# Performance work log

Hardware: AMD Instinct MI355X
Metric: run time of the kernel (lower is better)

## Reference

```python
import jax, jax.numpy as jnp
import numpy as np

B, T, E = 2, 4096, 1024
H = 16
D = E // H  # head_len = 64


def setup_inputs() -> dict:
    key = jax.random.key(0)
    ks = jax.random.split(key, 6)
    s = 1.0 / np.sqrt(E)
    return {
        "x": jax.random.normal(ks[0], (B, T, E), dtype=jnp.float32),
        # torch nn.Linear weights: shape (out, in), y = x @ W.T
        "Wq": jax.random.uniform(ks[1], (E, E), jnp.float32, -s, s),
        "Wk": jax.random.uniform(ks[2], (E, E), jnp.float32, -s, s),
        "Wv": jax.random.uniform(ks[3], (E, E), jnp.float32, -s, s),
        "Wo": jax.random.uniform(ks[4], (E, E), jnp.float32, -s, s),
        "bo": jax.random.uniform(ks[5], (E,), jnp.float32, -s, s),
    }


def reference(x, Wq, Wk, Wv, Wo, bo):
    Bx, Tx, Ex = x.shape
    q = x @ Wq.T
    k = x @ Wk.T
    v = x @ Wv.T
    # (B, T, H, D) -> (B, H, T, D)
    q = q.reshape(Bx, Tx, H, D).transpose(0, 2, 1, 3)
    k = k.reshape(Bx, Tx, H, D).transpose(0, 2, 1, 3)
    v = v.reshape(Bx, Tx, H, D).transpose(0, 2, 1, 3)
    # scores: (B, H, T, T), scaled by sqrt(head_len)
    sim = jnp.einsum("bhqd,bhkd->bhqk", q, k) / jnp.sqrt(jnp.float32(D))
    causal = jnp.tril(jnp.ones((Tx, Tx), dtype=bool))  # True = keep
    sim = jnp.where(causal[None, None], sim, -jnp.inf)
    attn = jax.nn.softmax(sim, axis=-1)
    # dropout_rate = 0.0 (eval) -> identity
    out = jnp.einsum("bhqk,bhkd->bhqd", attn, v)
    out = out.transpose(0, 2, 1, 3).reshape(Bx, Tx, Ex)
    return out @ Wo.T + bo
```

## Files before the change

kernel.cpp:

```cpp
#include <hip/hip_runtime.h>

typedef unsigned short bf16_t;
typedef __bf16 bf16x8 __attribute__((ext_vector_type(8)));
typedef float  v4f   __attribute__((ext_vector_type(4)));

__device__ __forceinline__ bf16_t f2bf(float f) {
    union { float f; unsigned u; } a; a.f = f;
    unsigned r = a.u + 0x7FFFu + ((a.u >> 16) & 1u);
    return (bf16_t)(r >> 16);
}
__device__ __forceinline__ bf16_t f2bf_trunc(float f) {
    union { float f; unsigned u; } a; a.f = f;
    return (bf16_t)(a.u >> 16);
}

#define GL16(g, l) __builtin_amdgcn_global_load_lds( \
    (__attribute__((address_space(1))) void*)(g),    \
    (__attribute__((address_space(3))) void*)(l), 16, 0, 0)

#define QSCALE 0.18033688011f

__global__ __launch_bounds__(256) void cvt_all(
    const float4* __restrict__ x,  const float4* __restrict__ wq,
    const float4* __restrict__ wk, const float4* __restrict__ wv,
    const float4* __restrict__ wo,
    ushort4* __restrict__ xb, ushort4* __restrict__ wqkv, ushort4* __restrict__ wob) {
    int i = blockIdx.x * 256 + threadIdx.x;
    const float4* s; ushort4* d; int off;
    if (i < 2097152) { s = x; d = xb; off = i; }
    else {
        int wdx = (i - 2097152) >> 18;
        off = (i - 2097152) & 262143;
        if      (wdx == 0) { s = wq; d = wqkv; }
        else if (wdx == 1) { s = wk; d = wqkv + 262144; }
        else if (wdx == 2) { s = wv; d = wqkv + 524288; }
        else               { s = wo; d = wob; }
    }
    float4 v = s[off];
    ushort4 o;
    o.x = f2bf(v.x); o.y = f2bf(v.y); o.z = f2bf(v.z); o.w = f2bf(v.w);
    d[off] = o;
}

#define GEMM_MAINLOOP(A_, W_)                                                          \
    __shared__ bf16_t As[128 * 32];                                                    \
    __shared__ bf16_t Bs[128 * 32];                                                    \
    const int tid = threadIdx.x;                                                       \
    const int w = tid >> 6, lane = tid & 63;                                           \
    const int lrow = lane & 15, lq = lane >> 4;                                        \
    const int m0 = blockIdx.y * 128, n0 = blockIdx.x * 128;                            \
    const int srow = w * 16 + (lane >> 2);                                             \
    const int sk = (lane & 3) * 8;                                                     \
    const int wm = (w & 1) * 64, wn = (w >> 1) * 64;                                   \
    v4f acc[4][4];                                                                     \
    _Pragma("unroll") for (int i = 0; i < 4; ++i)                                      \
        _Pragma("unroll") for (int j = 0; j < 4; ++j)                                  \
            acc[i][j] = (v4f){0.f, 0.f, 0.f, 0.f};                                     \
    for (int k0 = 0; k0 < 1024; k0 += 32) {                                            \
        __syncthreads();                                                               \
        GL16(A_ + (size_t)(m0 + srow) * 1024 + k0 + sk,      (char*)As + w * 1024);    \
        GL16(A_ + (size_t)(m0 + 64 + srow) * 1024 + k0 + sk, (char*)As + 4096 + w * 1024); \
        GL16(W_ + (size_t)(n0 + srow) * 1024 + k0 + sk,      (char*)Bs + w * 1024);    \
        GL16(W_ + (size_t)(n0 + 64 + srow) * 1024 + k0 + sk, (char*)Bs + 4096 + w * 1024); \
        __syncthreads();                                                               \
        bf16x8 af[4], bf[4];                                                           \
        _Pragma("unroll") for (int i = 0; i < 4; ++i)                                  \
            af[i] = *(const bf16x8*)&As[(wm + i * 16 + lrow) * 32 + lq * 8];           \
        _Pragma("unroll") for (int j = 0; j < 4; ++j)                                  \
            bf[j] = *(const bf16x8*)&Bs[(wn + j * 16 + lrow) * 32 + lq * 8];           \
        _Pragma("unroll") for (int i = 0; i < 4; ++i)                                  \
            _Pragma("unroll") for (int j = 0; j < 4; ++j)                              \
                acc[i][j] = __builtin_amdgcn_mfma_f32_16x16x32_bf16(af[i], bf[j],      \
                                                                    acc[i][j], 0, 0, 0); \
    }

__global__ __launch_bounds__(256) void gemm_qkv_kernel(
    const bf16_t* __restrict__ A, const bf16_t* __restrict__ W,
    bf16_t* __restrict__ Qb, bf16_t* __restrict__ Kb, bf16_t* __restrict__ Vtb) {
    GEMM_MAINLOOP(A, W)
#pragma unroll
    for (int i = 0; i < 4; ++i)
#pragma unroll
        for (int j = 0; j < 4; ++j)
#pragma unroll
            for (int r = 0; r < 4; ++r) {
                int m = m0 + wm + i * 16 + lq * 4 + r;
                int n = n0 + wn + j * 16 + lrow;
                float v = acc[i][j][r];
                int b = m >> 12, t = m & 4095;
                if (n < 1024) {
                    int h = n >> 6, d = n & 63;
                    Qb[(((size_t)b * 16 + h) * 4096 + t) * 64 + d] = f2bf(v * QSCALE);
                } else if (n < 2048) {
                    int nn = n - 1024, h = nn >> 6, d = nn & 63;
                    Kb[(((size_t)b * 16 + h) * 4096 + t) * 64 + d] = f2bf(v);
                } else {
                    int nn = n - 2048, h = nn >> 6, d = nn & 63;
                    Vtb[(((size_t)b * 16 + h) * 64 + d) * 4096 + t] = f2bf(v);
                }
            }
}

__global__ __launch_bounds__(256) void gemm_out_kernel(
    const bf16_t* __restrict__ A, const bf16_t* __restrict__ W,
    const float* __restrict__ bo, float* __restrict__ out) {
    GEMM_MAINLOOP(A, W)
#pragma unroll
    for (int j = 0; j < 4; ++j) {
        int n = n0 + wn + j * 16 + lrow;
        float bias = bo[n];
#pragma unroll
        for (int i = 0; i < 4; ++i)
#pragma unroll
            for (int r = 0; r < 4; ++r) {
                int m = m0 + wm + i * 16 + lq * 4 + r;
                out[(size_t)m * 1024 + n] = acc[i][j][r] + bias;
            }
    }
}

__global__ __launch_bounds__(256, 2) void attn_kernel(
    const bf16_t* __restrict__ Q, const bf16_t* __restrict__ K,
    const bf16_t* __restrict__ Vt, bf16_t* __restrict__ O) {
    __shared__ bf16_t Kls[2][2][64 * 32];
    __shared__ bf16_t Vls[2][2][64 * 32];
    __shared__ bf16_t Plds[4][32 * 64];
    const int tid = threadIdx.x;
    const int w = tid >> 6, lane = tid & 63;
    const int lrow = lane & 15, lq = lane >> 4;
    const int bh = blockIdx.y;
    const int g = blockIdx.x;

    const bf16_t* Qh = Q + (size_t)bh * (4096 * 64);
    const bf16_t* Kh = K + (size_t)bh * (4096 * 64);
    const bf16_t* Vh = Vt + (size_t)bh * (64 * 4096);
    bf16_t* Pw = Plds[w];
    const int b = bh >> 4, h = bh & 15;

    const int srow = lane >> 2;
    const int soff = (lane & 3) * 8;

    bf16x8 ones;
#pragma unroll
    for (int i = 0; i < 8; ++i) ones[i] = (__bf16)1.0f;

#pragma unroll 1
    for (int mem = 0; mem < 2; ++mem) {
        const int j = mem ? (31 - g) : g;
        const int q0 = j * 128;
        const int q0w = q0 + w * 32;
        const int nt = 2 * j + 2;
        const int wlast = 2 * j + (w >> 1);

        bf16x8 qf[2][2];
#pragma unroll
        for (int sub = 0; sub < 2; ++sub)
#pragma unroll
            for (int dk = 0; dk < 2; ++dk)
                qf[sub][dk] = *(const bf16x8*)&Qh[(size_t)(q0w + sub * 16 + lrow) * 64 + dk * 32 + lq * 8];

        v4f oacc[2][4];
        v4f lacc[2];
#pragma unroll
        for (int s2 = 0; s2 < 2; ++s2) {
            lacc[s2] = (v4f){0.f, 0.f, 0.f, 0.f};
#pragma unroll
            for (int d = 0; d < 4; ++d) oacc[s2][d] = (v4f){0.f, 0.f, 0.f, 0.f};
        }

        auto stage = [&](int kt, int buf) {
            const int kc0 = kt << 6;
#pragma unroll
            for (int i = 0; i < 2; ++i) {
                int idx = w * 2 + i;
                int half = idx >> 2, rg = idx & 3;
                GL16(Kh + (size_t)(kc0 + rg * 16 + srow) * 64 + half * 32 + soff,
                     (char*)&Kls[buf][half][rg * 512]);
                GL16(Vh + (size_t)(rg * 16 + srow) * 4096 + kc0 + half * 32 + soff,
                     (char*)&Vls[buf][half][rg * 512]);
            }
        };

        stage(0, 0);
        for (int kt = 0; kt < nt; ++kt) {
            const int buf = kt & 1;
            __syncthreads();
            if (kt + 1 < nt) stage(kt + 1, buf ^ 1);
            if (kt > wlast) continue;
            const int kc0 = kt << 6;

            bf16x8 kf0[4], kf1[4];
#pragma unroll
            for (int c = 0; c < 4; ++c) {
                kf0[c] = *(const bf16x8*)&Kls[buf][0][(c * 16 + lrow) * 32 + lq * 8];
                kf1[c] = *(const bf16x8*)&Kls[buf][1][(c * 16 + lrow) * 32 + lq * 8];
            }
            bf16x8 vf[4][2];
#pragma unroll
            for (int d = 0; d < 4; ++d)
#pragma unroll
                for (int kh = 0; kh < 2; ++kh)
                    vf[d][kh] = *(const bf16x8*)&Vls[buf][kh][(d * 16 + lrow) * 32 + lq * 8];

            v4f s[2][4];
#pragma unroll
            for (int sub = 0; sub < 2; ++sub)
#pragma unroll
                for (int c = 0; c < 4; ++c) {
                    v4f t0 = (v4f){0.f, 0.f, 0.f, 0.f};
                    t0 = __builtin_amdgcn_mfma_f32_16x16x32_bf16(qf[sub][0], kf0[c], t0, 0, 0, 0);
                    s[sub][c] = __builtin_amdgcn_mfma_f32_16x16x32_bf16(qf[sub][1], kf1[c], t0, 0, 0, 0);
                }

            if (kt == wlast) {
#pragma unroll
                for (int sub = 0; sub < 2; ++sub)
#pragma unroll
                    for (int c = 0; c < 4; ++c)
#pragma unroll
                        for (int r = 0; r < 4; ++r) {
                            int row = q0w + sub * 16 + lq * 4 + r;
                            int col = kc0 + c * 16 + lrow;
                            float p = __builtin_amdgcn_exp2f(s[sub][c][r]);
                            p = (col > row) ? 0.f : p;
                            Pw[(sub * 16 + lq * 4 + r) * 64 + ((c * 16 + lrow) ^ (lq * 16))] = f2bf_trunc(p);
                        }
            } else {
#pragma unroll
                for (int sub = 0; sub < 2; ++sub)
#pragma unroll
                    for (int c = 0; c < 4; ++c)
#pragma unroll
                        for (int r = 0; r < 4; ++r) {
                            float p = __builtin_amdgcn_exp2f(s[sub][c][r]);
                            Pw[(sub * 16 + lq * 4 + r) * 64 + ((c * 16 + lrow) ^ (lq * 16))] = f2bf_trunc(p);
                        }
            }

            bf16x8 pf[2][2];
#pragma unroll
            for (int sub = 0; sub < 2; ++sub)
#pragma unroll
                for (int kh = 0; kh < 2; ++kh)
                    pf[sub][kh] = *(const bf16x8*)&Pw[(sub * 16 + lrow) * 64 +
                                                      ((kh * 32 + lq * 8) ^ ((lrow >> 2) * 16))];

#pragma unroll
            for (int kh = 0; kh < 2; ++kh) {
#pragma unroll
                for (int sub = 0; sub < 2; ++sub)
                    lacc[sub] = __builtin_amdgcn_mfma_f32_16x16x32_bf16(pf[sub][kh], ones, lacc[sub], 0, 0, 0);
#pragma unroll
                for (int d = 0; d < 4; ++d) {
                    oacc[0][d] = __builtin_amdgcn_mfma_f32_16x16x32_bf16(pf[0][kh], vf[d][kh], oacc[0][d], 0, 0, 0);
                    oacc[1][d] = __builtin_amdgcn_mfma_f32_16x16x32_bf16(pf[1][kh], vf[d][kh], oacc[1][d], 0, 0, 0);
                }
            }
        }

#pragma unroll
        for (int sub = 0; sub < 2; ++sub) {
            float rl[4];
#pragma unroll
            for (int r = 0; r < 4; ++r) rl[r] = 1.0f / lacc[sub][r];
#pragma unroll
            for (int d = 0; d < 4; ++d)
#pragma unroll
                for (int r = 0; r < 4; ++r) {
                    int t = q0w + sub * 16 + lq * 4 + r;
                    O[((size_t)b * 4096 + t) * 1024 + h * 64 + d * 16 + lrow] =
                        f2bf(oacc[sub][d][r] * rl[r]);
                }
        }
    }
}

extern "C" void kernel_launch(void* const* d_in, const int* in_sizes, int n_in,
                              void* d_out, int out_size, void* d_ws, size_t ws_size,
                              hipStream_t stream) {
    const float* x  = (const float*)d_in[0];
    const float* Wq = (const float*)d_in[1];
    const float* Wk = (const float*)d_in[2];
    const float* Wv = (const float*)d_in[3];
    const float* Wo = (const float*)d_in[4];
    const float* bo = (const float*)d_in[5];
    float* out = (float*)d_out;

    char* ws = (char*)d_ws;
    bf16_t* xb   = (bf16_t*)(ws + 0);
    bf16_t* Wqkv = (bf16_t*)(ws + 16777216);
    bf16_t* Wob  = (bf16_t*)(ws + 23068672);
    bf16_t* Qb   = (bf16_t*)(ws + 25165824);
    bf16_t* Kb   = (bf16_t*)(ws + 41943040);
    bf16_t* Vtb  = (bf16_t*)(ws + 58720256);
    bf16_t* Ob   = (bf16_t*)(ws + 75497472);

    cvt_all<<<12288, 256, 0, stream>>>((const float4*)x, (const float4*)Wq,
                                       (const float4*)Wk, (const float4*)Wv,
                                       (const float4*)Wo,
                                       (ushort4*)xb, (ushort4*)Wqkv, (ushort4*)Wob);

    gemm_qkv_kernel<<<dim3(24, 64), 256, 0, stream>>>(xb, Wqkv, Qb, Kb, Vtb);

    attn_kernel<<<dim3(16, 32), 256, 0, stream>>>(Qb, Kb, Vtb, Ob);

    gemm_out_kernel<<<dim3(8, 64), 256, 0, stream>>>(Ob, Wob, bo, out);
}
```

Before: 326.2 us.

## Swizzle LDS layouts, transpose S tile, and stage V^T writes via LDS

The QKV GEMM epilogue is split per output type. The V^T portion is now transposed through shared memory with a swizzled layout and written with coalesced 16-byte stores, replacing strided scalar stores. In attention, K/V shared-memory reads and the staging offset are XOR-swizzled to cut bank conflicts. S is computed transposed (K as the A operand) so each lane packs 4 contiguous P values into one 8-byte LDS write instead of 16 scalar writes, and S/P work is done per sub-tile to reduce register pressure. This adds extra barriers in the V epilogue, and the consistency of the staging swizzle cannot be fully checked because the stage code is not visible.

```diff
diff --git a/kernel.cpp b/kernel.cpp
--- a/kernel.cpp
+++ b/kernel.cpp
@@ -9,9 +9,11 @@
     unsigned r = a.u + 0x7FFFu + ((a.u >> 16) & 1u);
     return (bf16_t)(r >> 16);
 }
-__device__ __forceinline__ bf16_t f2bf_trunc(float f) {
-    union { float f; unsigned u; } a; a.f = f;
-    return (bf16_t)(a.u >> 16);
+__device__ __forceinline__ unsigned fbits(float f) {
+    union { float f; unsigned u; } a; a.f = f; return a.u;
+}
+__device__ __forceinline__ unsigned pk_trunc(float lo, float hi) {
+    return (fbits(lo) >> 16) | (fbits(hi) & 0xFFFF0000u);
 }
 
 #define GL16(g, l) __builtin_amdgcn_global_load_lds( \
@@ -43,8 +45,8 @@
 }
 
 #define GEMM_MAINLOOP(A_, W_)                                                          \
-    __shared__ bf16_t As[128 * 32];                                                    \
-    __shared__ bf16_t Bs[128 * 32];                                                    \
+    __shared__ bf16_t SMEM[8192];                                                      \
+    bf16_t* As = SMEM; bf16_t* Bs = SMEM + 4096;                                       \
     const int tid = threadIdx.x;                                                       \
     const int w = tid >> 6, lane = tid & 63;                                           \
     const int lrow = lane & 15, lq = lane >> 4;                                        \
@@ -78,27 +80,62 @@
     const bf16_t* __restrict__ A, const bf16_t* __restrict__ W,
     bf16_t* __restrict__ Qb, bf16_t* __restrict__ Kb, bf16_t* __restrict__ Vtb) {
     GEMM_MAINLOOP(A, W)
-#pragma unroll
-    for (int i = 0; i < 4; ++i)
-#pragma unroll
-        for (int j = 0; j < 4; ++j)
-#pragma unroll
-            for (int r = 0; r < 4; ++r) {
-                int m = m0 + wm + i * 16 + lq * 4 + r;
-                int n = n0 + wn + j * 16 + lrow;
-                float v = acc[i][j][r];
-                int b = m >> 12, t = m & 4095;
-                if (n < 1024) {
+    const int x = blockIdx.x;
+    const int b = m0 >> 12, t0 = m0 & 4095;
+    if (x < 8) {
+#pragma unroll
+        for (int i = 0; i < 4; ++i)
+#pragma unroll
+            for (int j = 0; j < 4; ++j)
+#pragma unroll
+                for (int r = 0; r < 4; ++r) {
+                    int t = t0 + wm + i * 16 + lq * 4 + r;
+                    int n = n0 + wn + j * 16 + lrow;
                     int h = n >> 6, d = n & 63;
-                    Qb[(((size_t)b * 16 + h) * 4096 + t) * 64 + d] = f2bf(v * QSCALE);
-                } else if (n < 2048) {
-                    int nn = n - 1024, h = nn >> 6, d = nn & 63;
-                    Kb[(((size_t)b * 16 + h) * 4096 + t) * 64 + d] = f2bf(v);
-                } else {
-                    int nn = n - 2048, h = nn >> 6, d = nn & 63;
-                    Vtb[(((size_t)b * 16 + h) * 64 + d) * 4096 + t] = f2bf(v);
-                }
-            }
+                    Qb[(((size_t)b * 16 + h) * 4096 + t) * 64 + d] =
+                        f2bf(acc[i][j][r] * QSCALE);
+                }
+    } else if (x < 16) {
+#pragma unroll
+        for (int i = 0; i < 4; ++i)
+#pragma unroll
+            for (int j = 0; j < 4; ++j)
+#pragma unroll
+                for (int r = 0; r < 4; ++r) {
+                    int t = t0 + wm + i * 16 + lq * 4 + r;
+                    int nn = n0 + wn + j * 16 + lrow - 1024;
+                    int h = nn >> 6, d = nn & 63;
+                    Kb[(((size_t)b * 16 + h) * 4096 + t) * 64 + d] = f2bf(acc[i][j][r]);
+                }
+    } else {
+        const int d0 = n0 - 2048;
+#pragma unroll 1
+        for (int p = 0; p < 2; ++p) {
+            __syncthreads();
+            if ((w >> 1) == p) {
+#pragma unroll
+                for (int i = 0; i < 4; ++i)
+#pragma unroll
+                    for (int j = 0; j < 4; ++j) {
+                        int row = j * 16 + lrow;
+                        int swz = (row & 7) << 1;
+                        int g = (wm >> 2) + i * 4 + lq;
+                        uint2 u;
+                        u.x = (unsigned)f2bf(acc[i][j][0]) | ((unsigned)f2bf(acc[i][j][1]) << 16);
+                        u.y = (unsigned)f2bf(acc[i][j][2]) | ((unsigned)f2bf(acc[i][j][3]) << 16);
+                        *(uint2*)&SMEM[row * 128 + ((g ^ swz) << 2)] = u;
+                    }
+            }
+            __syncthreads();
+#pragma unroll
+            for (int uu = 0; uu < 4; ++uu) {
+                int unit = tid + 256 * uu;
+                int row = unit >> 4, seg = unit & 15;
+                uint4 val = *(const uint4*)&SMEM[row * 128 + ((seg ^ (row & 7)) << 3)];
+                *(uint4*)&Vtb[((size_t)b * 1024 + d0 + p * 64 + row) * 4096 + t0 + seg * 8] = val;
+            }
+        }
+    }
 }
 
 __global__ __launch_bounds__(256) void gemm_out_kernel(
@@ -138,7 +175,9 @@
     const int b = bh >> 4, h = bh & 15;
 
     const int srow = lane >> 2;
-    const int soff = (lane & 3) * 8;
+    const int soff = (((lane & 3) ^ (srow & 3))) * 8;
+    const int kswz = (lq ^ (lrow & 3)) * 8;
+    const int pswz = (lrow & 7) << 1;
 
     bf16x8 ones;
 #pragma unroll
@@ -188,72 +227,65 @@
             if (kt + 1 < nt) stage(kt + 1, buf ^ 1);
             if (kt > wlast) continue;
             const int kc0 = kt << 6;
+            const bool diag = (kt == wlast);
 
             bf16x8 kf0[4], kf1[4];
 #pragma unroll
             for (int c = 0; c < 4; ++c) {
-                kf0[c] = *(const bf16x8*)&Kls[buf][0][(c * 16 + lrow) * 32 + lq * 8];
-                kf1[c] = *(const bf16x8*)&Kls[buf][1][(c * 16 + lrow) * 32 + lq * 8];
+                kf0[c] = *(const bf16x8*)&Kls[buf][0][(c * 16 + lrow) * 32 + kswz];
+                kf1[c] = *(const bf16x8*)&Kls[buf][1][(c * 16 + lrow) * 32 + kswz];
             }
             bf16x8 vf[4][2];
 #pragma unroll
             for (int d = 0; d < 4; ++d)
 #pragma unroll
                 for (int kh = 0; kh < 2; ++kh)
-                    vf[d][kh] = *(const bf16x8*)&Vls[buf][kh][(d * 16 + lrow) * 32 + lq * 8];
-
-            v4f s[2][4];
-#pragma unroll
-            for (int sub = 0; sub < 2; ++sub)
+                    vf[d][kh] = *(const bf16x8*)&Vls[buf][kh][(d * 16 + lrow) * 32 + kswz];
+
+#pragma unroll
+            for (int sub = 0; sub < 2; ++sub) {
+                const int qrow = sub * 16 + lrow;
+                const int qglob = q0w + qrow;
+
+                v4f st[4];
 #pragma unroll
                 for (int c = 0; c < 4; ++c) {
-                    v4f t0 = (v4f){0.f, 0.f, 0.f, 0.f};
-                    t0 = __builtin_amdgcn_mfma_f32_16x16x32_bf16(qf[sub][0], kf0[c], t0, 0, 0, 0);
-                    s[sub][c] = __builtin_amdgcn_mfma_f32_16x16x32_bf16(qf[sub][1], kf1[c], t0, 0, 0, 0);
-                }
-
-            if (kt == wlast) {
-#pragma unroll
-                for (int sub = 0; sub < 2; ++sub)
-#pragma unroll
-                    for (int c = 0; c < 4; ++c)
-#pragma unroll
-                        for (int r = 0; r < 4; ++r) {
-                            int row = q0w + sub * 16 + lq * 4 + r;
-                            int col = kc0 + c * 16 + lrow;
-                            float p = __builtin_amdgcn_exp2f(s[sub][c][r]);
-                            p = (col > row) ? 0.f : p;
-                            Pw[(sub * 16 + lq * 4 + r) * 64 + ((c * 16 + lrow) ^ (lq * 16))] = f2bf_trunc(p);
+                    v4f t0v = (v4f){0.f, 0.f, 0.f, 0.f};
+                    t0v = __builtin_amdgcn_mfma_f32_16x16x32_bf16(kf0[c], qf[sub][0], t0v, 0, 0, 0);
+                    st[c] = __builtin_amdgcn_mfma_f32_16x16x32_bf16(kf1[c], qf[sub][1], t0v, 0, 0, 0);
+                }
+
+#pragma unroll
+                for (int c = 0; c < 4; ++c) {
+                    float p[4];
+#pragma unroll
+                    for (int r = 0; r < 4; ++r) {
+                        float pv = __builtin_amdgcn_exp2f(st[c][r]);
+                        if (diag) {
+                            int tg = kc0 + c * 16 + lq * 4 + r;
+                            pv = (tg > qglob) ? 0.f : pv;
                         }
-            } else {
-#pragma unroll
-                for (int sub = 0; sub < 2; ++sub)
-#pragma unroll
-                    for (int c = 0; c < 4; ++c)
-#pragma unroll
-                        for (int r = 0; r < 4; ++r) {
-                            float p = __builtin_amdgcn_exp2f(s[sub][c][r]);
-                            Pw[(sub * 16 + lq * 4 + r) * 64 + ((c * 16 + lrow) ^ (lq * 16))] = f2bf_trunc(p);
-                        }
-            }
-
-            bf16x8 pf[2][2];
-#pragma unroll
-            for (int sub = 0; sub < 2; ++sub)
-#pragma unroll
-                for (int kh = 0; kh < 2; ++kh)
-                    pf[sub][kh] = *(const bf16x8*)&Pw[(sub * 16 + lrow) * 64 +
-                                                      ((kh * 32 + lq * 8) ^ ((lrow >> 2) * 16))];
-
-#pragma unroll
-            for (int kh = 0; kh < 2; ++kh) {
-#pragma unroll
-                for (int sub = 0; sub < 2; ++sub)
-                    lacc[sub] = __builtin_amdgcn_mfma_f32_16x16x32_bf16(pf[sub][kh], ones, lacc[sub], 0, 0, 0);
-#pragma unroll
-                for (int d = 0; d < 4; ++d) {
-                    oacc[0][d] = __builtin_amdgcn_mfma_f32_16x16x32_bf16(pf[0][kh], vf[d][kh], oacc[0][d], 0, 0, 0);
-                    oacc[1][d] = __builtin_amdgcn_mfma_f32_16x16x32_bf16(pf[1][kh], vf[d][kh], oacc[1][d], 0, 0, 0);
+                        p[r] = pv;
+                    }
+                    uint2 u;
+                    u.x = pk_trunc(p[0], p[1]);
+                    u.y = pk_trunc(p[2], p[3]);
+                    *(uint2*)&Pw[qrow * 64 + (((c * 4 + lq) ^ pswz) << 2)] = u;
+                }
+
+                bf16x8 pf[2];
+#pragma unroll
+                for (int kh = 0; kh < 2; ++kh) {
+                    int s0 = kh * 8 + lq * 2;
+                    pf[kh] = *(const bf16x8*)&Pw[qrow * 64 + ((s0 ^ pswz) << 2)];
+                }
+
+#pragma unroll
+                for (int kh = 0; kh < 2; ++kh) {
+                    lacc[sub] = __builtin_amdgcn_mfma_f32_16x16x32_bf16(pf[kh], ones, lacc[sub], 0, 0, 0);
+#pragma unroll
+                    for (int d = 0; d < 4; ++d)
+                        oacc[sub][d] = __builtin_amdgcn_mfma_f32_16x16x32_bf16(pf[kh], vf[d][kh], oacc[sub][d], 0, 0, 0);
                 }
             }
         }
```

Result: faster. 316.0 us (-3.1%).
